# Optimization experiments

Hardware: AMD Instinct MI355X
Metric: run time of the kernel (lower is better)

The kernel has to match this reference:

```python
import jax, jax.numpy as jnp
import numpy as np

BLOCKS = 16
TEMP = 0.7
SINK_ITERS = 8
CUT = 8
GUMBEL_EPS = 1e-6
IN_EPS = 1e-5
NEG = -1e9  # stands in for log(0) = -inf; exp(NEG) == 0 in fp32, avoids nan grads


def setup_inputs() -> dict:
    key = jax.random.key(0)
    k1, k2, k3 = jax.random.split(key, 3)
    shape = (8, 512, 4096, 1)  # [B, C, H, W=1]
    return {
        "q": jax.random.normal(k1, shape, jnp.float32),
        "k": jax.random.normal(k2, shape, jnp.float32),
        "v": jax.random.normal(k3, shape, jnp.float32),
    }


def _block_cat(x, blocks):
    # torch: cat(x.chunk(blocks, dim=2)[:-1], dim=-1)
    # [B,C,H,W] -> [B,C,H/blocks,(blocks-1)*W]
    B, C, H, W = x.shape
    Hb = H // blocks
    xb = x.reshape(B, C, blocks, Hb, W)[:, :, : blocks - 1]  # drop last chunk
    return jnp.transpose(xb, (0, 1, 3, 2, 4)).reshape(B, C, Hb, (blocks - 1) * W)


def reference(q, k, v):
    B, C, H, W = q.shape
    Hb = H // BLOCKS
    N = BLOCKS - 1  # number of retained blocks

    b_q = _block_cat(q, BLOCKS)  # [B,C,Hb,N]
    b_k = _block_cat(k, BLOCKS)
    b_v = _block_cat(v, BLOCKS)

    # ---- AttentionPermMatrix: Gumbel-Sinkhorn soft permutation [B,N,N] ----
    sq = jnp.swapaxes(b_q.mean(axis=1), 1, 2)  # [B,N,Hb]
    sk = jnp.swapaxes(b_k.mean(axis=1), 1, 2)
    R = jnp.einsum('bie,bje->bij', sq, sk) * (C ** -0.5)  # [B,N,N]
    Rp = jax.nn.relu(R)
    pos = R > 0
    r = jnp.where(pos, jnp.log(jnp.where(pos, Rp, 1.0)), NEG)  # safe log(relu(R))
    u = jax.random.uniform(jax.random.key(42), r.shape, r.dtype)
    gumbel = -jnp.log(-jnp.log(u + GUMBEL_EPS) + GUMBEL_EPS)
    r = (r + gumbel) / TEMP
    for _ in range(SINK_ITERS):
        r = r - jax.nn.logsumexp(r, axis=2, keepdims=True)
        r = r - jax.nn.logsumexp(r, axis=1, keepdims=True)
    perm = jnp.exp(r)  # [B,N,N]

    # ---- permute blocks of k/v (perm broadcast over channel dim C) ----
    k_sort = jnp.einsum('bchn,bnm->bchm', b_k, perm)  # [B,C,Hb,N]
    v_sort = jnp.einsum('bchn,bnm->bchm', b_v, perm)

    # ---- cut: first CUT size-1 chunks along last dim, cat along dim=-2, transpose(1,3)
    def cut(x):
        # [B,C,Hb,N] -> [B,C,CUT*Hb,1] (chunk j occupies rows j*Hb:(j+1)*Hb) -> [B,1,CUT*Hb,C]
        xc = jnp.transpose(x[..., :CUT], (0, 1, 3, 2)).reshape(B, C, CUT * Hb, 1)
        return jnp.transpose(xc, (0, 3, 2, 1))

    k_cut = cut(k_sort)  # [B,1,M,C], M = CUT*Hb
    v_cut = cut(v_sort)
    q_t = jnp.transpose(q, (0, 3, 2, 1))  # [B,1,H,C]

    logits = jnp.einsum('bwhc,bwmc->bwhm', q_t, k_cut) / TEMP  # [B,1,H,M]
    attn = jax.nn.softmax(logits, axis=-1)
    val = jnp.einsum('bwhm,bwmc->bwhc', attn, v_cut)  # [B,1,H,C]

    # InstanceNorm2d (affine=False): normalize over spatial dims (2,3) per (B, channel)
    mu = val.mean(axis=(2, 3), keepdims=True)
    var = val.var(axis=(2, 3), keepdims=True)
    return (val - mu) / jnp.sqrt(var + IN_EPS)
```

## Files before the change

### kernel.cpp

```cpp
#include <hip/hip_runtime.h>
#include <stdint.h>

typedef _Float16 half_t;
typedef _Float16 half8 __attribute__((ext_vector_type(8)));
typedef float floatx4 __attribute__((ext_vector_type(4)));

#define B_ 8
#define C_ 512
#define H_ 4096
#define HB 256
#define NB 15
#define CUT_ 8
#define M_ 2048
#define INV_TEMP (1.0f/0.7f)
#define NEG (-1e9f)

#define KROW 528
#define KT_BYTES 33792u
#define VT_BYTES 32768u

#define SQ_OFFB   0u
#define SK_OFFB   122880u
#define ST_OFFB   245760u
#define PERM_OFFB 245824u
#define KC16_OFFB 262144u
#define VC16_OFFB (262144u + 17301504u)
#define WS_NEED   (262144u + 17301504u + 16777216u)

__device__ __forceinline__ unsigned rotl32(unsigned x, unsigned n) {
    return (x << n) | (x >> (32u - n));
}
__device__ __forceinline__ void threefry2x32(unsigned k0, unsigned k1,
                                             unsigned x0, unsigned x1,
                                             unsigned &o0, unsigned &o1) {
    unsigned k2 = 0x1BD11BDAu ^ k0 ^ k1;
    x0 += k0; x1 += k1;
    x0+=x1; x1=rotl32(x1,13); x1^=x0;
    x0+=x1; x1=rotl32(x1,15); x1^=x0;
    x0+=x1; x1=rotl32(x1,26); x1^=x0;
    x0+=x1; x1=rotl32(x1, 6); x1^=x0;
    x0+=k1; x1+=k2+1u;
    x0+=x1; x1=rotl32(x1,17); x1^=x0;
    x0+=x1; x1=rotl32(x1,29); x1^=x0;
    x0+=x1; x1=rotl32(x1,16); x1^=x0;
    x0+=x1; x1=rotl32(x1,24); x1^=x0;
    x0+=k2; x1+=k0+2u;
    x0+=x1; x1=rotl32(x1,13); x1^=x0;
    x0+=x1; x1=rotl32(x1,15); x1^=x0;
    x0+=x1; x1=rotl32(x1,26); x1^=x0;
    x0+=x1; x1=rotl32(x1, 6); x1^=x0;
    x0+=k0; x1+=k1+3u;
    x0+=x1; x1=rotl32(x1,17); x1^=x0;
    x0+=x1; x1=rotl32(x1,29); x1^=x0;
    x0+=x1; x1=rotl32(x1,16); x1^=x0;
    x0+=x1; x1=rotl32(x1,24); x1^=x0;
    x0+=k1; x1+=k2+4u;
    x0+=x1; x1=rotl32(x1,13); x1^=x0;
    x0+=x1; x1=rotl32(x1,15); x1^=x0;
    x0+=x1; x1=rotl32(x1,26); x1^=x0;
    x0+=x1; x1=rotl32(x1, 6); x1^=x0;
    x0+=k2; x1+=k0+5u;
    o0 = x0; o1 = x1;
}

__device__ __forceinline__ void stage_tile8(const char* gsrc, char* lbase,
                                            int w, int lane, int nchunk) {
    #pragma unroll
    for (int i = 0; i < 5; i++) {
        int cc = w + 8*i;
        if (cc < nchunk) {
            __builtin_amdgcn_global_load_lds(
                (const __attribute__((address_space(1))) void*)(uintptr_t)
                    (gsrc + (size_t)cc*1024u + (size_t)lane*16u),
                (__attribute__((address_space(3))) void*)(uintptr_t)
                    (lbase + (size_t)cc*1024u),
                16, 0, 0);
        }
    }
}

__global__ void colmean_kernel(const float* __restrict__ q, const float* __restrict__ k,
                               float* __restrict__ sq, float* __restrict__ sk) {
    int id  = blockIdx.x * 256 + threadIdx.x;
    int h   = id % 3840;
    int rest= id / 3840;
    int b   = rest % 8;
    int seg = rest / 8;
    int c0  = seg * 64;
    const float* qb = q + ((size_t)b*C_ + c0) * H_ + h;
    const float* kb = k + ((size_t)b*C_ + c0) * H_ + h;
    float aq = 0.f, ak = 0.f;
    #pragma unroll 8
    for (int c = 0; c < 64; c++) {
        aq += qb[(size_t)c * H_];
        ak += kb[(size_t)c * H_];
    }
    atomicAdd(&sq[b*3840 + h], aq * (1.0f/512.0f));
    atomicAdd(&sk[b*3840 + h], ak * (1.0f/512.0f));
}

__global__ void perm_kernel(const float* __restrict__ sqg, const float* __restrict__ skg,
                            float* __restrict__ perm) {
    int b = blockIdx.x;
    int tid = threadIdx.x;
    __shared__ float sqs[NB*HB];
    __shared__ float sks[NB*HB];
    __shared__ float mat[NB][16];
    __shared__ float lse[NB];
    for (int i = tid; i < NB*HB; i += 256) {
        sqs[i] = sqg[b*3840 + i];
        sks[i] = skg[b*3840 + i];
    }
    __syncthreads();
    int i = tid / 15, j = tid % 15;
    if (tid < 225) {
        float acc = 0.f;
        for (int h = 0; h < HB; h++) acc += sqs[i*HB + h] * sks[j*HB + h];
        float R = acc * 0.044194173824159216f;
        float r0 = (R > 0.0f) ? logf(R) : NEG;
        int g = (b*15 + i)*15 + j;
        unsigned o0, o1;
        threefry2x32(0u, 42u, 0u, (unsigned)g, o0, o1);
        unsigned bits = o0 ^ o1;
        float u = __uint_as_float((bits >> 9) | 0x3f800000u) - 1.0f;
        float gum = -logf(-logf(u + 1e-6f) + 1e-6f);
        mat[i][j] = (r0 + gum) * INV_TEMP;
    }
    __syncthreads();
    for (int it = 0; it < 8; it++) {
        if (tid < 15) {
            float m = -3.4e38f;
            for (int jj = 0; jj < 15; jj++) m = fmaxf(m, mat[tid][jj]);
            float s = 0.f;
            for (int jj = 0; jj < 15; jj++) s += expf(mat[tid][jj] - m);
            lse[tid] = m + logf(s);
        }
        __syncthreads();
        if (tid < 225) mat[i][j] -= lse[i];
        __syncthreads();
        if (tid < 15) {
            float m = -3.4e38f;
            for (int ii = 0; ii < 15; ii++) m = fmaxf(m, mat[ii][tid]);
            float s = 0.f;
            for (int ii = 0; ii < 15; ii++) s += expf(mat[ii][tid] - m);
            lse[tid] = m + logf(s);
        }
        __syncthreads();
        if (tid < 225) mat[i][j] -= lse[j];
        __syncthreads();
    }
    if (tid < 225) perm[b*225 + tid] = expf(mat[i][j]);
}

__global__ __launch_bounds__(256)
void kcut_kernel(const float* __restrict__ k, const float* __restrict__ perm,
                 half_t* __restrict__ kc) {
    int bid  = blockIdx.x;
    int ct   = bid & 7;
    int chalf= (bid >> 3) & 1;
    int hch  = (bid >> 4) & 7;
    int b    = bid >> 7;
    int h0 = hch * 32;
    int tid = threadIdx.x;
    __shared__ float kt[32*481];
    __shared__ float pl[NB][CUT_];
    if (tid < NB*CUT_) pl[tid/CUT_][tid%CUT_] = perm[b*225 + (tid/CUT_)*15 + (tid%CUT_)];
    int cp = tid & 31;
    int hg = tid >> 5;
    int c0 = chalf*256 + ct*32;
    for (int it = 0; it < 15; it++) {
        int slot = tid + it*256;
        int h4 = slot & 7;
        int n  = (slot >> 3) % 15;
        int cc = slot / 120;
        float4 vv = *(const float4*)&k[((size_t)(b*C_ + c0 + cc))*H_ + n*HB + h0 + h4*4];
        *(float4*)&kt[cc*481 + n*32 + h4*4] = vv;
    }
    __syncthreads();
    float acc[CUT_][4];
    #pragma unroll
    for (int j = 0; j < CUT_; j++) { acc[j][0]=0.f; acc[j][1]=0.f; acc[j][2]=0.f; acc[j][3]=0.f; }
    #pragma unroll
    for (int n = 0; n < NB; n++) {
        float kv0 = kt[cp*481 + n*32 + hg*4 + 0];
        float kv1 = kt[cp*481 + n*32 + hg*4 + 1];
        float kv2 = kt[cp*481 + n*32 + hg*4 + 2];
        float kv3 = kt[cp*481 + n*32 + hg*4 + 3];
        #pragma unroll
        for (int j = 0; j < CUT_; j++) {
            float p = pl[n][j];
            acc[j][0] += kv0*p; acc[j][1] += kv1*p; acc[j][2] += kv2*p; acc[j][3] += kv3*p;
        }
    }
    #pragma unroll
    for (int j = 0; j < CUT_; j++)
        for (int q2 = 0; q2 < 4; q2++) {
            int m = j*HB + h0 + hg*4 + q2;
            kc[(((size_t)b*64 + (m>>5))*32 + (m&31))*KROW + c0 + cp] = (half_t)acc[j][q2];
        }
}

__global__ __launch_bounds__(256)
void vcut_kernel(const float* __restrict__ v, const float* __restrict__ perm,
                 half_t* __restrict__ vc) {
    int bc = blockIdx.x;
    int b = bc >> 9;
    int c = bc & 511;
    int h = threadIdx.x;
    __shared__ float pl[NB][CUT_];
    if (h < NB*CUT_) pl[h/CUT_][h%CUT_] = perm[b*225 + (h/CUT_)*15 + (h%CUT_)];
    __syncthreads();
    const float* vb = v + (size_t)bc * H_ + h;
    float av[CUT_] = {0,0,0,0,0,0,0,0};
    #pragma unroll
    for (int n = 0; n < NB; n++) {
        float vv = vb[n*HB];
        #pragma unroll
        for (int j = 0; j < CUT_; j++) av[j] += vv * pl[n][j];
    }
    #pragma unroll
    for (int j = 0; j < CUT_; j++)
        vc[(((size_t)b*64 + j*8 + (h>>5))*512 + c)*32 + (h&31)] = (half_t)av[j];
}

__global__ __launch_bounds__(512, 2)
void attn_kernel(const float* __restrict__ q, const half_t* __restrict__ kc,
                 const half_t* __restrict__ vc, float* __restrict__ out,
                 float* __restrict__ stats) {
    __shared__ half_t ktile[2][32][KROW];
    __shared__ half_t vtile[512][40];
    __shared__ float  spart[2][32][68];
    __shared__ half_t pslab[2][64][40];
    __shared__ float  redbuf[8][2];

    int bid = blockIdx.x;
    int b   = bid & 7;
    int h0  = (bid >> 3) * 64;
    int tid = threadIdx.x;
    int w    = tid >> 6;
    int lane = tid & 63;
    int lm   = lane & 15;
    int quad = lane >> 4;
    int wm = w & 3;
    int wc = w >> 2;
    int row = 16*wm + lm;
    int key0 = 4*quad;

    const char* kbytes = (const char*)kc + (size_t)b * 64u * KT_BYTES;
    const char* vbytes = (const char*)vc + (size_t)b * 64u * VT_BYTES;

    stage_tile8(kbytes, (char*)&ktile[0][0][0], w, lane, 33);

    float (*qstage)[68] = reinterpret_cast<float(*)[68]>(&spart[0][0][0]);

    half8 qhi[8], qlo[8];
    for (int ch = 0; ch < 8; ch++) {
        int c0 = ch * 64;
        asm volatile("s_waitcnt lgkmcnt(0)\n\ts_barrier" ::: "memory");
        #pragma unroll
        for (int it = 0; it < 2; it++) {
            int slot = tid + it*512;
            int cc = slot >> 4;
            int h4 = slot & 15;
            float4 qv = *(const float4*)&q[((size_t)(b*C_ + c0 + cc))*H_ + h0 + h4*4];
            qstage[h4*4+0][cc] = qv.x;
            qstage[h4*4+1][cc] = qv.y;
            qstage[h4*4+2][cc] = qv.z;
            qstage[h4*4+3][cc] = qv.w;
        }
        asm volatile("s_waitcnt lgkmcnt(0)\n\ts_barrier" ::: "memory");
        if ((ch >> 2) == wc) {
            #pragma unroll
            for (int kk = 0; kk < 2; kk++) {
                int kb = (ch & 3)*2 + kk;
                const float* qp = &qstage[row][kk*32 + quad*8];
                float4 a = *(const float4*)qp;
                float4 c4 = *(const float4*)(qp + 4);
                float vals[8] = {a.x,a.y,a.z,a.w,c4.x,c4.y,c4.z,c4.w};
                half8 hh, hl;
                #pragma unroll
                for (int j = 0; j < 8; j++) {
                    float xv = vals[j] * INV_TEMP;
                    half_t h1 = (half_t)xv;
                    hh[j] = h1;
                    hl[j] = (half_t)(xv - (float)h1);
                }
                qhi[kb] = hh; qlo[kb] = hl;
            }
        }
    }

    floatx4 O[16];
    #pragma unroll
    for (int n = 0; n < 16; n++) O[n] = (floatx4)0.f;
    floatx4 Ol = (floatx4)0.f;
    float ms = -3.4e38f;
    half8 vone;
    #pragma unroll
    for (int j = 0; j < 8; j++) vone[j] = (half_t)1.0f;

    int buf = 0;
    for (int t = 0; t < 64; t++) {
        __syncthreads();
        float4 vst[4];
        {
            const half_t* vt = (const half_t*)(vbytes + (size_t)t*VT_BYTES);
            #pragma unroll
            for (int i = 0; i < 4; i++) vst[i] = *(const float4*)(vt + tid*32 + i*8);
        }
        if (t + 1 < 64)
            stage_tile8(kbytes + (size_t)(t+1)*KT_BYTES, (char*)&ktile[buf^1][0][0], w, lane, 33);

        floatx4 acc0 = (floatx4)0.f, acc1 = (floatx4)0.f;
        __builtin_amdgcn_s_setprio(1);
        #pragma unroll
        for (int kb = 0; kb < 8; kb++) {
            int coff = 256*wc + 32*kb + quad*8;
            half8 a0 = *(const half8*)&ktile[buf][lm][coff];
            half8 a1 = *(const half8*)&ktile[buf][16 + lm][coff];
            acc0 = __builtin_amdgcn_mfma_f32_16x16x32_f16(a0, qhi[kb], acc0, 0, 0, 0);
            acc0 = __builtin_amdgcn_mfma_f32_16x16x32_f16(a0, qlo[kb], acc0, 0, 0, 0);
            acc1 = __builtin_amdgcn_mfma_f32_16x16x32_f16(a1, qhi[kb], acc1, 0, 0, 0);
            acc1 = __builtin_amdgcn_mfma_f32_16x16x32_f16(a1, qlo[kb], acc1, 0, 0, 0);
        }
        __builtin_amdgcn_s_setprio(0);
        #pragma unroll
        for (int i = 0; i < 4; i++) *(float4*)&vtile[tid][i*8] = vst[i];
        #pragma unroll
        for (int r = 0; r < 4; r++) {
            spart[wc][key0 + r][row]      = acc0[r];
            spart[wc][16 + key0 + r][row] = acc1[r];
        }
        asm volatile("s_waitcnt lgkmcnt(0)\n\ts_barrier" ::: "memory");

        float s0[4], s1[4];
        #pragma unroll
        for (int r = 0; r < 4; r++) {
            s0[r] = acc0[r] + spart[wc^1][key0 + r][row];
            s1[r] = acc1[r] + spart[wc^1][16 + key0 + r][row];
        }
        float m2 = fmaxf(fmaxf(fmaxf(s0[0],s0[1]), fmaxf(s0[2],s0[3])),
                         fmaxf(fmaxf(s1[0],s1[1]), fmaxf(s1[2],s1[3])));
        m2 = fmaxf(m2, __shfl_xor(m2, 16, 64));
        m2 = fmaxf(m2, __shfl_xor(m2, 32, 64));
        int need = (m2 > ms + 8.0f) ? 1 : 0;
        if (__any(need)) {
            float mn = fmaxf(ms, m2);
            float aown = __expf(ms - mn);
            ms = mn;
            float ar[4];
            #pragma unroll
            for (int r = 0; r < 4; r++) ar[r] = __shfl(aown, key0 + r, 64);
            #pragma unroll
            for (int r = 0; r < 4; r++) Ol[r] *= ar[r];
            #pragma unroll
            for (int n = 0; n < 16; n++) {
                #pragma unroll
                for (int r = 0; r < 4; r++) O[n][r] *= ar[r];
            }
        }
        #pragma unroll
        for (int r = 0; r < 4; r++) {
            pslab[wc][row][key0 + r]      = (half_t)__expf(s0[r] - ms);
            pslab[wc][row][16 + key0 + r] = (half_t)__expf(s1[r] - ms);
        }
        half8 pa = *(const half8*)&pslab[wc][row][quad*8];
        __builtin_amdgcn_s_setprio(1);
        #pragma unroll
        for (int n = 0; n < 16; n++) {
            half8 vb = *(const half8*)&vtile[256*wc + 16*n + lm][quad*8];
            O[n] = __builtin_amdgcn_mfma_f32_16x16x32_f16(pa, vb, O[n], 0, 0, 0);
        }
        Ol = __builtin_amdgcn_mfma_f32_16x16x32_f16(pa, vone, Ol, 0, 0, 0);
        __builtin_amdgcn_s_setprio(0);
        buf ^= 1;
    }

    float inv4[4];
    #pragma unroll
    for (int r = 0; r < 4; r++) inv4[r] = 1.0f / Ol[r];
    float sa = 0.f, sb = 0.f;
    int rowg = h0 + 16*wm + quad*4;
    #pragma unroll
    for (int n = 0; n < 16; n++) {
        #pragma unroll
        for (int r = 0; r < 4; r++) {
            float o = O[n][r] * inv4[r];
            out[((size_t)b*H_ + rowg + r)*C_ + 256*wc + 16*n + lm] = o;
            sa += o; sb += o*o;
        }
    }
    #pragma unroll
    for (int msk = 1; msk < 64; msk <<= 1) {
        sa += __shfl_xor(sa, msk, 64);
        sb += __shfl_xor(sb, msk, 64);
    }
    if (lane == 0) { redbuf[w][0] = sa; redbuf[w][1] = sb; }
    __syncthreads();
    if (tid == 0) {
        float a = 0.f, c2 = 0.f;
        for (int w2 = 0; w2 < 8; w2++) { a += redbuf[w2][0]; c2 += redbuf[w2][1]; }
        atomicAdd(&stats[b*2    ], a);
        atomicAdd(&stats[b*2 + 1], c2);
    }
}

__global__ void norm_kernel(float* __restrict__ out, const float* __restrict__ stats) {
    size_t i = (size_t)blockIdx.x * 256 + threadIdx.x;
    int b = (int)(i >> 19);
    float4 vv = ((float4*)out)[i];
    const float inv = 1.0f / (4096.0f * 512.0f);
    float mu  = stats[b*2] * inv;
    float var = stats[b*2 + 1] * inv - mu*mu;
    float rs  = rsqrtf(var + 1e-5f);
    vv.x = (vv.x - mu) * rs;
    vv.y = (vv.y - mu) * rs;
    vv.z = (vv.z - mu) * rs;
    vv.w = (vv.w - mu) * rs;
    ((float4*)out)[i] = vv;
}

extern "C" void kernel_launch(void* const* d_in, const int* in_sizes, int n_in,
                              void* d_out, int out_size, void* d_ws, size_t ws_size,
                              hipStream_t stream) {
    const float* q = (const float*)d_in[0];
    const float* k = (const float*)d_in[1];
    const float* v = (const float*)d_in[2];
    float* out = (float*)d_out;
    if (ws_size < (size_t)WS_NEED) return;

    float*  sq    = (float*) ((char*)d_ws + SQ_OFFB);
    float*  sk    = (float*) ((char*)d_ws + SK_OFFB);
    float*  stats = (float*) ((char*)d_ws + ST_OFFB);
    float*  perm  = (float*) ((char*)d_ws + PERM_OFFB);
    half_t* kc    = (half_t*)((char*)d_ws + KC16_OFFB);
    half_t* vc    = (half_t*)((char*)d_ws + VC16_OFFB);

    hipMemsetAsync(d_ws, 0, (size_t)KC16_OFFB, stream);

    colmean_kernel<<<960,  256, 0, stream>>>(q, k, sq, sk);
    perm_kernel   <<<8,    256, 0, stream>>>(sq, sk, perm);
    kcut_kernel   <<<1024, 256, 0, stream>>>(k, perm, kc);
    vcut_kernel   <<<4096, 256, 0, stream>>>(v, perm, vc);
    attn_kernel   <<<512,  512, 0, stream>>>(q, kc, vc, out, stats);
    norm_kernel   <<<16384,256, 0, stream>>>(out, stats);
}
```

Before: 567.6 us.

## Load V fragments directly into registers and swizzle K tile to cut LDS conflicts

V tiles are no longer staged through shared memory; each wave loads its MFMA B-operand fragments straight from global memory into 16 half8 registers. The K-cut layout is XOR-swizzled at write time and the LDS reads use the matching swizzle to avoid bank conflicts, while the score partial-sum exchange and P slab writes are changed to vectorized row-major stores. This removes one LDS round trip per tile and reduces LDS traffic, at the cost of many more live registers, which may spill or lower occupancy under launch_bounds(512,2).

```diff
diff --git a/kernel.cpp b/kernel.cpp
--- a/kernel.cpp
+++ b/kernel.cpp
@@ -2,6 +2,7 @@
 #include <stdint.h>
 
 typedef _Float16 half_t;
+typedef _Float16 half4 __attribute__((ext_vector_type(4)));
 typedef _Float16 half8 __attribute__((ext_vector_type(8)));
 typedef float floatx4 __attribute__((ext_vector_type(4)));
 
@@ -192,11 +193,12 @@
             acc[j][0] += kv0*p; acc[j][1] += kv1*p; acc[j][2] += kv2*p; acc[j][3] += kv3*p;
         }
     }
+    int cs = c0 + (cp ^ (8*(hg & 3)));
     #pragma unroll
     for (int j = 0; j < CUT_; j++)
         for (int q2 = 0; q2 < 4; q2++) {
             int m = j*HB + h0 + hg*4 + q2;
-            kc[(((size_t)b*64 + (m>>5))*32 + (m&31))*KROW + c0 + cp] = (half_t)acc[j][q2];
+            kc[(((size_t)b*64 + (m>>5))*32 + (m&31))*KROW + cs] = (half_t)acc[j][q2];
         }
 }
 
@@ -228,8 +230,7 @@
                  const half_t* __restrict__ vc, float* __restrict__ out,
                  float* __restrict__ stats) {
     __shared__ half_t ktile[2][32][KROW];
-    __shared__ half_t vtile[512][40];
-    __shared__ float  spart[2][32][68];
+    __shared__ float  spart[2][64][36];
     __shared__ half_t pslab[2][64][40];
     __shared__ float  redbuf[8][2];
 
@@ -245,6 +246,7 @@
     int wc = w >> 2;
     int row = 16*wm + lm;
     int key0 = 4*quad;
+    int sxk = 8*((lm >> 2) & 3);
 
     const char* kbytes = (const char*)kc + (size_t)b * 64u * KT_BYTES;
     const char* vbytes = (const char*)vc + (size_t)b * 64u * VT_BYTES;
@@ -302,11 +304,12 @@
     int buf = 0;
     for (int t = 0; t < 64; t++) {
         __syncthreads();
-        float4 vst[4];
+        half8 vreg[16];
         {
             const half_t* vt = (const half_t*)(vbytes + (size_t)t*VT_BYTES);
             #pragma unroll
-            for (int i = 0; i < 4; i++) vst[i] = *(const float4*)(vt + tid*32 + i*8);
+            for (int n = 0; n < 16; n++)
+                vreg[n] = *(const half8*)(vt + (256*wc + 16*n + lm)*32 + quad*8);
         }
         if (t + 1 < 64)
             stage_tile8(kbytes + (size_t)(t+1)*KT_BYTES, (char*)&ktile[buf^1][0][0], w, lane, 33);
@@ -315,7 +318,7 @@
         __builtin_amdgcn_s_setprio(1);
         #pragma unroll
         for (int kb = 0; kb < 8; kb++) {
-            int coff = 256*wc + 32*kb + quad*8;
+            int coff = (256*wc + 32*kb + quad*8) ^ sxk;
             half8 a0 = *(const half8*)&ktile[buf][lm][coff];
             half8 a1 = *(const half8*)&ktile[buf][16 + lm][coff];
             acc0 = __builtin_amdgcn_mfma_f32_16x16x32_f16(a0, qhi[kb], acc0, 0, 0, 0);
@@ -324,20 +327,17 @@
             acc1 = __builtin_amdgcn_mfma_f32_16x16x32_f16(a1, qlo[kb], acc1, 0, 0, 0);
         }
         __builtin_amdgcn_s_setprio(0);
-        #pragma unroll
-        for (int i = 0; i < 4; i++) *(float4*)&vtile[tid][i*8] = vst[i];
+        *(floatx4*)&spart[wc][row][key0]      = acc0;
+        *(floatx4*)&spart[wc][row][16 + key0] = acc1;
+        asm volatile("s_waitcnt lgkmcnt(0)\n\ts_barrier" ::: "memory");
+
+        floatx4 pp0 = *(const floatx4*)&spart[wc^1][row][key0];
+        floatx4 pp1 = *(const floatx4*)&spart[wc^1][row][16 + key0];
+        float s0[4], s1[4];
         #pragma unroll
         for (int r = 0; r < 4; r++) {
-            spart[wc][key0 + r][row]      = acc0[r];
-            spart[wc][16 + key0 + r][row] = acc1[r];
-        }
-        asm volatile("s_waitcnt lgkmcnt(0)\n\ts_barrier" ::: "memory");
-
-        float s0[4], s1[4];
-        #pragma unroll
-        for (int r = 0; r < 4; r++) {
-            s0[r] = acc0[r] + spart[wc^1][key0 + r][row];
-            s1[r] = acc1[r] + spart[wc^1][16 + key0 + r][row];
+            s0[r] = acc0[r] + pp0[r];
+            s1[r] = acc1[r] + pp1[r];
         }
         float m2 = fmaxf(fmaxf(fmaxf(s0[0],s0[1]), fmaxf(s0[2],s0[3])),
                          fmaxf(fmaxf(s1[0],s1[1]), fmaxf(s1[2],s1[3])));
@@ -359,18 +359,19 @@
                 for (int r = 0; r < 4; r++) O[n][r] *= ar[r];
             }
         }
+        half4 hp0, hp1;
         #pragma unroll
         for (int r = 0; r < 4; r++) {
-            pslab[wc][row][key0 + r]      = (half_t)__expf(s0[r] - ms);
-            pslab[wc][row][16 + key0 + r] = (half_t)__expf(s1[r] - ms);
-        }
+            hp0[r] = (half_t)__expf(s0[r] - ms);
+            hp1[r] = (half_t)__expf(s1[r] - ms);
+        }
+        *(half4*)&pslab[wc][row][key0]      = hp0;
+        *(half4*)&pslab[wc][row][16 + key0] = hp1;
         half8 pa = *(const half8*)&pslab[wc][row][quad*8];
         __builtin_amdgcn_s_setprio(1);
         #pragma unroll
-        for (int n = 0; n < 16; n++) {
-            half8 vb = *(const half8*)&vtile[256*wc + 16*n + lm][quad*8];
-            O[n] = __builtin_amdgcn_mfma_f32_16x16x32_f16(pa, vb, O[n], 0, 0, 0);
-        }
+        for (int n = 0; n < 16; n++)
+            O[n] = __builtin_amdgcn_mfma_f32_16x16x32_f16(pa, vreg[n], O[n], 0, 0, 0);
         Ol = __builtin_amdgcn_mfma_f32_16x16x32_f16(pa, vone, Ol, 0, 0, 0);
         __builtin_amdgcn_s_setprio(0);
         buf ^= 1;
```

New measurement: 653.9 us. 1.15x slower.
